# Performance work log

Measured on AMD Instinct MI355X. Metric: run time of the kernel, lower is better.

## Reference

```python
import jax, jax.numpy as jnp
import numpy as np

N_NODES = 50000
N_EDGES = 600000
IN_DIM = 128
HID = 128
OUT_DIM = 2
N_GRAPHS = 64
EPS = 1e-12  # F.normalize default eps


def setup_inputs() -> dict:
    key = jax.random.key(0)
    ks = jax.random.split(key, 16)
    s = 0.05
    x = jax.random.normal(ks[0], (N_NODES, IN_DIM), jnp.float32)
    edge_index = jax.random.randint(ks[1], (2, N_EDGES), 0, N_NODES, dtype=jnp.int32)
    batch = jnp.sort(jax.random.randint(ks[2], (N_NODES,), 0, N_GRAPHS, dtype=jnp.int32))
    # GraphSage layer 0: lin (IN->HID), agg_lin (IN+HID -> HID)
    lin_w0 = jax.random.normal(ks[3], (IN_DIM, HID), jnp.float32) * s
    lin_b0 = jnp.zeros((HID,), jnp.float32)
    agg_w0 = jax.random.normal(ks[4], (HID + IN_DIM, HID), jnp.float32) * s
    agg_b0 = jnp.zeros((HID,), jnp.float32)
    # GraphSage layer 1: lin (HID->HID), agg_lin (2*HID -> HID)
    lin_w1 = jax.random.normal(ks[5], (HID, HID), jnp.float32) * s
    lin_b1 = jnp.zeros((HID,), jnp.float32)
    agg_w1 = jax.random.normal(ks[6], (2 * HID, HID), jnp.float32) * s
    agg_b1 = jnp.zeros((HID,), jnp.float32)
    # post_mp: Linear(HID,HID) -> Dropout -> Linear(HID,OUT)
    mp_w1 = jax.random.normal(ks[7], (HID, HID), jnp.float32) * s
    mp_b1 = jnp.zeros((HID,), jnp.float32)
    mp_w2 = jax.random.normal(ks[8], (HID, OUT_DIM), jnp.float32) * s
    mp_b2 = jnp.zeros((OUT_DIM,), jnp.float32)
    return dict(x=x, edge_index=edge_index, batch=batch,
                lin_w0=lin_w0, lin_b0=lin_b0, agg_w0=agg_w0, agg_b0=agg_b0,
                lin_w1=lin_w1, lin_b1=lin_b1, agg_w1=agg_w1, agg_b1=agg_b1,
                mp_w1=mp_w1, mp_b1=mp_b1, mp_w2=mp_w2, mp_b2=mp_b2)


def sage_layer(x, lin_w, lin_b, agg_w, agg_b, src, dst, num_nodes):
    # message: ReLU(Linear(x_j)) gathered along source nodes  [E, HID]
    msg = jax.nn.relu(x[src] @ lin_w + lin_b)
    # aggr='mean' scatter to target nodes
    summed = jax.ops.segment_sum(msg, dst, num_segments=num_nodes)
    deg = jax.ops.segment_sum(jnp.ones((src.shape[0], 1), x.dtype), dst,
                              num_segments=num_nodes)
    agg = summed / jnp.maximum(deg, 1.0)
    # update: ReLU(Linear([aggr, x])) then L2-normalize rows
    h = jax.nn.relu(jnp.concatenate([agg, x], axis=-1) @ agg_w + agg_b)
    norm = jnp.sqrt(jnp.sum(h * h, axis=1, keepdims=True))
    return h / jnp.maximum(norm, EPS)


def reference(x, edge_index, batch,
              lin_w0, lin_b0, agg_w0, agg_b0,
              lin_w1, lin_b1, agg_w1, agg_b1,
              mp_w1, mp_b1, mp_w2, mp_b2):
    src, dst = edge_index[0], edge_index[1]
    n = x.shape[0]
    h = sage_layer(x, lin_w0, lin_b0, agg_w0, agg_b0, src, dst, n)
    # F.relu is a no-op on the non-negative normalized output; dropout p=0 -> identity
    h = sage_layer(h, lin_w1, lin_b1, agg_w1, agg_b1, src, dst, n)
    # global max pool over graphs
    pooled = jax.ops.segment_max(h, batch, num_segments=N_GRAPHS)
    pooled = jnp.where(jnp.isfinite(pooled), pooled, 0.0)  # guard empty graphs
    # post_mp: Linear -> Dropout(identity) -> Linear
    z = (pooled @ mp_w1 + mp_b1) @ mp_w2 + mp_b2
    return jax.nn.log_softmax(z, axis=1)
```

## Files before the change

### kernel.cpp

```cpp
#include <hip/hip_runtime.h>

__device__ __forceinline__ float bf2f(ushort u) {
    union { uint i; float f; } c; c.i = ((uint)u) << 16; return c.f;
}
__device__ __forceinline__ ushort f2bf(float f) {
    union { float f; uint i; } c; c.f = f;
    uint b = c.i;
    uint r = (b + 0x7fffu + ((b >> 16) & 1u)) >> 16;
    return (ushort)r;
}

typedef __bf16 v8bf __attribute__((ext_vector_type(8)));
typedef float  v4f  __attribute__((ext_vector_type(4)));

__global__ __launch_bounds__(256) void sniff_kernel(const uint* __restrict__ words, int* __restrict__ flag) {
    __shared__ int s[256];
    int t = threadIdx.x;
    int bad = 0;
    for (int i = t; i < 2048; i += 256) {
        uint w = words[i];
        uint exp = (w >> 7) & 0xffu;
        if (exp >= 143u) bad++;
    }
    s[t] = bad;
    __syncthreads();
    for (int o = 128; o; o >>= 1) {
        if (t < o) s[t] += s[t + o];
        __syncthreads();
    }
    if (t == 0) *flag = (s[0] > 64) ? 1 : 0;
}

__device__ __forceinline__ ushort load_conv(const void* src, int i, int isf32) {
    return isf32 ? f2bf(((const float*)src)[i]) : ((const ushort*)src)[i];
}

__global__ __launch_bounds__(256) void convert_x8(const void* __restrict__ src, ushort* __restrict__ dst,
                                                  int n, const int* __restrict__ flag) {
    int idx = blockIdx.x * 256 + threadIdx.x;
    int base = idx * 8;
    if (base + 8 <= n) {
        if (*flag) {
            const float4* s4 = (const float4*)src;
            float4 a = s4[idx * 2], b = s4[idx * 2 + 1];
            union { ushort u[8]; uint4 v; } o;
            o.u[0] = f2bf(a.x); o.u[1] = f2bf(a.y); o.u[2] = f2bf(a.z); o.u[3] = f2bf(a.w);
            o.u[4] = f2bf(b.x); o.u[5] = f2bf(b.y); o.u[6] = f2bf(b.z); o.u[7] = f2bf(b.w);
            *(uint4*)(dst + base) = o.v;
        } else {
            *(uint4*)(dst + base) = ((const uint4*)src)[idx];
        }
    } else {
        int isf = *flag;
        for (int i = base; i < n; i++) dst[i] = load_conv(src, i, isf);
    }
}

struct SmallSrcs { const void* p[8]; };
__global__ __launch_bounds__(256) void convert_small(SmallSrcs s, ushort* __restrict__ dst,
                                                     const int* __restrict__ flag) {
    const int offs[9] = {0, 128, 256, 384, 512, 16896, 17024, 17280, 17282};
    int idx = blockIdx.x * 256 + threadIdx.x;
    if (idx >= 17282) return;
    int seg = 0;
    while (idx >= offs[seg + 1]) seg++;
    dst[idx] = load_conv(s.p[seg], idx - offs[seg], *flag);
}

__global__ __launch_bounds__(256) void transpose_all(
    const void* __restrict__ w0, const void* __restrict__ wa0,
    const void* __restrict__ w1, const void* __restrict__ wa1,
    ushort* __restrict__ t0, ushort* __restrict__ ta0,
    ushort* __restrict__ t1, ushort* __restrict__ ta1,
    const int* __restrict__ flag) {
    int idx = blockIdx.x * 256 + threadIdx.x;
    const void* W; ushort* T; int K; int local;
    if (idx < 16384)      { W = w0;  T = t0;  K = 128; local = idx; }
    else if (idx < 49152) { W = wa0; T = ta0; K = 256; local = idx - 16384; }
    else if (idx < 65536) { W = w1;  T = t1;  K = 128; local = idx - 49152; }
    else                  { W = wa1; T = ta1; K = 256; local = idx - 65536; }
    ushort v = load_conv(W, local, *flag);
    int k = local >> 7;
    int n = local & 127;
    T[(size_t)n * K + k] = v;
}

__global__ __launch_bounds__(256) void count_deg(const int* __restrict__ dst, int* __restrict__ deg, int E) {
    int i = blockIdx.x * 256 + threadIdx.x;
    if (i < E) atomicAdd(&deg[dst[i]], 1);
}

#define SCAN_CHUNK 1024

__global__ __launch_bounds__(256) void chunk_sum_kernel(const int* __restrict__ deg,
                                                        int* __restrict__ csums, int n) {
    __shared__ int s[256];
    int t = threadIdx.x;
    int base = blockIdx.x * SCAN_CHUNK + t * 4;
    int v = 0;
    if (base + 4 <= n) {
        int4 q = *(const int4*)(deg + base);
        v = q.x + q.y + q.z + q.w;
    } else {
        for (int i = base; i < n; i++) v += deg[i];
    }
    s[t] = v;
    __syncthreads();
    for (int o = 128; o; o >>= 1) {
        if (t < o) s[t] += s[t + o];
        __syncthreads();
    }
    if (t == 0) csums[blockIdx.x] = s[0];
}

__global__ __launch_bounds__(256) void scan_phase2(const int* __restrict__ deg,
                                                   const int* __restrict__ csums,
                                                   int* __restrict__ rowptr, int* __restrict__ cursor,
                                                   int n) {
    __shared__ int red[256];
    int t = threadIdx.x, b = blockIdx.x;
    int v = 0;
    for (int i = t; i < b; i += 256) v += csums[i];
    red[t] = v;
    __syncthreads();
    for (int o = 128; o; o >>= 1) {
        if (t < o) red[t] += red[t + o];
        __syncthreads();
    }
    int chunkOff = red[0];
    __syncthreads();
    int base = b * SCAN_CHUNK + t * 4;
    int d0 = 0, d1 = 0, d2 = 0, d3 = 0;
    if (base + 4 <= n) {
        int4 q = *(const int4*)(deg + base);
        d0 = q.x; d1 = q.y; d2 = q.z; d3 = q.w;
    } else {
        if (base < n)     d0 = deg[base];
        if (base + 1 < n) d1 = deg[base + 1];
        if (base + 2 < n) d2 = deg[base + 2];
        if (base + 3 < n) d3 = deg[base + 3];
    }
    int s4 = d0 + d1 + d2 + d3;
    red[t] = s4;
    __syncthreads();
    for (int o = 1; o < 256; o <<= 1) {
        int u = (t >= o) ? red[t - o] : 0;
        __syncthreads();
        red[t] += u;
        __syncthreads();
    }
    int run = chunkOff + red[t] - s4;
    if (base < n)     { rowptr[base]     = run; cursor[base]     = run; run += d0; }
    if (base + 1 < n) { rowptr[base + 1] = run; cursor[base + 1] = run; run += d1; }
    if (base + 2 < n) { rowptr[base + 2] = run; cursor[base + 2] = run; run += d2; }
    if (base + 3 < n) { rowptr[base + 3] = run; cursor[base + 3] = run; run += d3; }
    if (n >= base && n < base + 4) rowptr[n] = run;
}

__global__ __launch_bounds__(256) void fill_kernel(const int* __restrict__ src, const int* __restrict__ dst,
                                                   int* __restrict__ cursor, int* __restrict__ csr_src, int E) {
    int i = blockIdx.x * 256 + threadIdx.x;
    if (i < E) {
        int pos = atomicAdd(&cursor[dst[i]], 1);
        csr_src[pos] = src[i];
    }
}

template <int NSTAGE, bool NORM>
__global__ __launch_bounds__(256) void gemm_kernel(
    const ushort* __restrict__ A0, const ushort* __restrict__ A1,
    const ushort* __restrict__ Bt, const ushort* __restrict__ bias,
    ushort* __restrict__ Cout, int M) {
    __shared__ __bf16 As[128 * 72];
    __shared__ __bf16 Bs[128 * 72];
    const int t = threadIdx.x;
    const int w = t >> 6, lane = t & 63, ln = lane & 15, q = lane >> 4;
    const int blockRow = blockIdx.x * 128;
    const int K = NSTAGE * 128;

    v4f acc[2][8];
#pragma unroll
    for (int i = 0; i < 2; i++)
#pragma unroll
        for (int j = 0; j < 8; j++) acc[i][j] = (v4f){0.f, 0.f, 0.f, 0.f};

    for (int kc = 0; kc < K; kc += 64) {
        const ushort* Ap = (kc < 128) ? A0 : A1;
        int kin = kc & 127;
#pragma unroll
        for (int i = 0; i < 4; i++) {
            int c = i * 256 + t;
            int row = c >> 3, c8 = c & 7;
            int grow = blockRow + row; if (grow >= M) grow = M - 1;
            *(uint4*)&As[row * 72 + c8 * 8] = *(const uint4*)(Ap + (size_t)grow * 128 + kin + c8 * 8);
            *(uint4*)&Bs[row * 72 + c8 * 8] = *(const uint4*)(Bt + (size_t)row * K + kc + c8 * 8);
        }
        __syncthreads();
#pragma unroll
        for (int k0 = 0; k0 < 64; k0 += 32) {
            v8bf a0 = *(const v8bf*)&As[(w * 32 + ln) * 72 + k0 + q * 8];
            v8bf a1 = *(const v8bf*)&As[(w * 32 + 16 + ln) * 72 + k0 + q * 8];
#pragma unroll
            for (int nt = 0; nt < 8; nt++) {
                v8bf b = *(const v8bf*)&Bs[(nt * 16 + ln) * 72 + k0 + q * 8];
                acc[0][nt] = __builtin_amdgcn_mfma_f32_16x16x32_bf16(a0, b, acc[0][nt], 0, 0, 0);
                acc[1][nt] = __builtin_amdgcn_mfma_f32_16x16x32_bf16(a1, b, acc[1][nt], 0, 0, 0);
            }
        }
        __syncthreads();
    }

    float biasf[8];
#pragma unroll
    for (int nt = 0; nt < 8; nt++) biasf[nt] = bf2f(bias[nt * 16 + ln]);

#pragma unroll
    for (int mt = 0; mt < 2; mt++) {
        float v[8][4];
#pragma unroll
        for (int nt = 0; nt < 8; nt++)
#pragma unroll
            for (int r = 0; r < 4; r++) {
                float x = acc[mt][nt][r] + biasf[nt];
                v[nt][r] = x > 0.f ? x : 0.f;
            }
        float inv[4];
        if (NORM) {
#pragma unroll
            for (int r = 0; r < 4; r++) {
                float p = 0.f;
#pragma unroll
                for (int nt = 0; nt < 8; nt++) p += v[nt][r] * v[nt][r];
                p += __shfl_xor(p, 1);
                p += __shfl_xor(p, 2);
                p += __shfl_xor(p, 4);
                p += __shfl_xor(p, 8);
                inv[r] = 1.0f / fmaxf(sqrtf(p), 1e-12f);
            }
        }
        int rowbase = blockRow + w * 32 + mt * 16 + q * 4;
#pragma unroll
        for (int r = 0; r < 4; r++) {
            int grow = rowbase + r;
            if (grow < M) {
#pragma unroll
                for (int nt = 0; nt < 8; nt++) {
                    float x = NORM ? v[nt][r] * inv[r] : v[nt][r];
                    Cout[(size_t)grow * 128 + nt * 16 + ln] = f2bf(x);
                }
            }
        }
    }
}

__global__ __launch_bounds__(256) void aggregate_kernel(
    const ushort* __restrict__ msg, const int* __restrict__ rowptr,
    const int* __restrict__ csr_src, ushort* __restrict__ agg, int n) {
    int wid = (int)((blockIdx.x * 256u + threadIdx.x) >> 6);
    int lane = threadIdx.x & 63;
    if (wid >= n) return;
    int start = rowptr[wid], end = rowptr[wid + 1];
    float a0 = 0.f, a1 = 0.f;
#pragma unroll 4
    for (int j = start; j < end; j++) {
        int s = csr_src[j];
        uint v = *(const uint*)(msg + (size_t)s * 128 + lane * 2);
        a0 += bf2f((ushort)(v & 0xffffu));
        a1 += bf2f((ushort)(v >> 16));
    }
    float inv = 1.0f / fmaxf((float)(end - start), 1.0f);
    uint o = (uint)f2bf(a0 * inv) | ((uint)f2bf(a1 * inv) << 16);
    *(uint*)(agg + (size_t)wid * 128 + lane * 2) = o;
}

__global__ __launch_bounds__(256) void pool_kernel(const ushort* __restrict__ h, const int* __restrict__ batch,
                                                   int* __restrict__ pooled, int n) {
    int d = threadIdx.x & 127;
    int half = threadIdx.x >> 7;
    int start = blockIdx.x * 128;
    int cur_b = -1;
    float cur_max = 0.f;
    for (int i = 0; i < 64; i++) {
        int node = start + half + i * 2;
        if (node >= n) break;
        int b = batch[node];
        float v = bf2f(h[(size_t)node * 128 + d]);
        if (b != cur_b) {
            if (cur_b >= 0) atomicMax(&pooled[cur_b * 128 + d], __float_as_int(cur_max));
            cur_b = b; cur_max = v;
        } else {
            cur_max = fmaxf(cur_max, v);
        }
    }
    if (cur_b >= 0) atomicMax(&pooled[cur_b * 128 + d], __float_as_int(cur_max));
}

__global__ __launch_bounds__(256) void final_kernel(const float* __restrict__ pooled,
                                                    const ushort* __restrict__ small,
                                                    void* __restrict__ out, int G,
                                                    const int* __restrict__ flag) {
    __shared__ float P[128];
    __shared__ float Thalf[128];
    __shared__ float T[128];
    __shared__ float R0[128], R1[128];
    const ushort* w1 = small + 512;
    const ushort* b1 = small + 16896;
    const ushort* w2 = small + 17024;
    const ushort* b2 = small + 17280;
    int g = blockIdx.x;
    int t = threadIdx.x;
    int j = t & 127, half = t >> 7;
    if (t < 128) P[t] = pooled[g * 128 + t];
    __syncthreads();
    float acc = 0.f;
    int k0 = half * 64;
#pragma unroll 8
    for (int k = k0; k < k0 + 64; k++) acc += P[k] * bf2f(w1[k * 128 + j]);
    if (half == 0) Thalf[j] = acc;
    __syncthreads();
    if (half == 1) T[j] = Thalf[j] + acc + bf2f(b1[j]);
    __syncthreads();
    if (t < 128) {
        float tv = T[t];
        R0[t] = tv * bf2f(w2[t * 2]);
        R1[t] = tv * bf2f(w2[t * 2 + 1]);
    }
    __syncthreads();
    for (int o = 64; o; o >>= 1) {
        if (t < o) { R0[t] += R0[t + o]; R1[t] += R1[t + o]; }
        __syncthreads();
    }
    if (t == 0) {
        float z0 = R0[0] + bf2f(b2[0]);
        float z1 = R1[0] + bf2f(b2[1]);
        float m = fmaxf(z0, z1);
        float l = m + logf(expf(z0 - m) + expf(z1 - m));
        float o0 = z0 - l, o1 = z1 - l;
        if (*flag) {
            ((float*)out)[2 * g]     = o0;
            ((float*)out)[2 * g + 1] = o1;
        } else {
            ((ushort*)out)[2 * g]     = f2bf(o0);
            ((ushort*)out)[2 * g + 1] = f2bf(o1);
        }
    }
}

extern "C" void kernel_launch(void* const* d_in, const int* in_sizes, int n_in,
                              void* d_out, int out_size, void* d_ws, size_t ws_size,
                              hipStream_t stream) {
    const void* x      = d_in[0];
    const int*  ei     = (const int*)d_in[1];
    const int*  batch  = (const int*)d_in[2];

    const int N = in_sizes[0] / 128;
    const int E = in_sizes[1] / 2;
    const int G = out_size / 2;
    const int* srcIdx = ei;
    const int* dstIdx = ei + E;

    char* ws = (char*)d_ws;
    size_t off = 0;
    auto alloc = [&](size_t bytes) -> void* {
        off = (off + 255) & ~(size_t)255;
        void* p = ws + off;
        off += bytes;
        return p;
    };
    int*    flag    = (int*)alloc(4);
    int*    deg     = (int*)alloc((size_t)N * 4);
    int*    rowptr  = (int*)alloc((size_t)(N + 1) * 4);
    int*    cursor  = (int*)alloc((size_t)N * 4);
    int*    csr_src = (int*)alloc((size_t)E * 4);
    int*    csums   = (int*)alloc(((size_t)N / SCAN_CHUNK + 2) * 4);
    ushort* Wt0     = (ushort*)alloc(128 * 128 * 2);
    ushort* WtA0    = (ushort*)alloc(256 * 128 * 2);
    ushort* Wt1     = (ushort*)alloc(128 * 128 * 2);
    ushort* WtA1    = (ushort*)alloc(256 * 128 * 2);
    ushort* small   = (ushort*)alloc(17282 * 2);
    ushort* xb      = (ushort*)alloc((size_t)N * 128 * 2);
    ushort* msg     = (ushort*)alloc((size_t)N * 128 * 2);
    ushort* agg     = (ushort*)alloc((size_t)N * 128 * 2);
    ushort* h0      = (ushort*)alloc((size_t)N * 128 * 2);
    int*    pooled  = (int*)alloc((size_t)G * 128 * 4);
    ushort* h1 = msg;

    sniff_kernel<<<1, 256, 0, stream>>>((const uint*)x, flag);
    convert_x8<<<(N * 128 + 2047) / 2048, 256, 0, stream>>>(x, xb, N * 128, flag);
    transpose_all<<<384, 256, 0, stream>>>(d_in[3], d_in[5], d_in[7], d_in[9],
                                           Wt0, WtA0, Wt1, WtA1, flag);
    SmallSrcs ss;
    ss.p[0] = d_in[4];  ss.p[1] = d_in[6];  ss.p[2] = d_in[8];  ss.p[3] = d_in[10];
    ss.p[4] = d_in[11]; ss.p[5] = d_in[12]; ss.p[6] = d_in[13]; ss.p[7] = d_in[14];
    convert_small<<<68, 256, 0, stream>>>(ss, small, flag);

    hipMemsetAsync(deg, 0, (size_t)N * 4, stream);
    int eb = (E + 255) / 256;
    count_deg<<<eb, 256, 0, stream>>>(dstIdx, deg, E);
    int nchunks = (N + SCAN_CHUNK - 1) / SCAN_CHUNK;
    chunk_sum_kernel<<<nchunks, 256, 0, stream>>>(deg, csums, N);
    scan_phase2<<<N / SCAN_CHUNK + 1, 256, 0, stream>>>(deg, csums, rowptr, cursor, N);
    fill_kernel<<<eb, 256, 0, stream>>>(srcIdx, dstIdx, cursor, csr_src, E);

    int gb = (N + 127) / 128;
    int ab = (N + 3) / 4;

    gemm_kernel<1, false><<<gb, 256, 0, stream>>>(xb, xb, Wt0, small + 0, msg, N);
    aggregate_kernel<<<ab, 256, 0, stream>>>(msg, rowptr, csr_src, agg, N);
    gemm_kernel<2, true><<<gb, 256, 0, stream>>>(agg, xb, WtA0, small + 128, h0, N);

    gemm_kernel<1, false><<<gb, 256, 0, stream>>>(h0, h0, Wt1, small + 256, msg, N);
    aggregate_kernel<<<ab, 256, 0, stream>>>(msg, rowptr, csr_src, agg, N);
    gemm_kernel<2, true><<<gb, 256, 0, stream>>>(agg, h0, WtA1, small + 384, h1, N);

    hipMemsetAsync(pooled, 0, (size_t)G * 128 * 4, stream);
    pool_kernel<<<(N + 127) / 128, 256, 0, stream>>>(h1, batch, pooled, N);
    final_kernel<<<G, 256, 0, stream>>>((const float*)pooled, small, d_out, G, flag);
}
```

Measured before the change: 324.3 us.

## Fuse max-pool into final GEMM, vectorize aggregation, merge weight prep kernels

```diff
diff --git a/kernel.cpp b/kernel.cpp
--- a/kernel.cpp
+++ b/kernel.cpp
@@ -2,6 +2,12 @@
 
 __device__ __forceinline__ float bf2f(ushort u) {
     union { uint i; float f; } c; c.i = ((uint)u) << 16; return c.f;
+}
+__device__ __forceinline__ float bf2lo(uint v) {
+    union { uint i; float f; } c; c.i = v << 16; return c.f;
+}
+__device__ __forceinline__ float bf2hi(uint v) {
+    union { uint i; float f; } c; c.i = v & 0xffff0000u; return c.f;
 }
 __device__ __forceinline__ ushort f2bf(float f) {
     union { float f; uint i; } c; c.f = f;
@@ -57,32 +63,32 @@
 }
 
 struct SmallSrcs { const void* p[8]; };
-__global__ __launch_bounds__(256) void convert_small(SmallSrcs s, ushort* __restrict__ dst,
-                                                     const int* __restrict__ flag) {
-    const int offs[9] = {0, 128, 256, 384, 512, 16896, 17024, 17280, 17282};
-    int idx = blockIdx.x * 256 + threadIdx.x;
-    if (idx >= 17282) return;
-    int seg = 0;
-    while (idx >= offs[seg + 1]) seg++;
-    dst[idx] = load_conv(s.p[seg], idx - offs[seg], *flag);
-}
-
-__global__ __launch_bounds__(256) void transpose_all(
+__global__ __launch_bounds__(256) void prep_weights(
     const void* __restrict__ w0, const void* __restrict__ wa0,
     const void* __restrict__ w1, const void* __restrict__ wa1,
     ushort* __restrict__ t0, ushort* __restrict__ ta0,
     ushort* __restrict__ t1, ushort* __restrict__ ta1,
+    SmallSrcs s, ushort* __restrict__ smalldst,
     const int* __restrict__ flag) {
     int idx = blockIdx.x * 256 + threadIdx.x;
-    const void* W; ushort* T; int K; int local;
-    if (idx < 16384)      { W = w0;  T = t0;  K = 128; local = idx; }
-    else if (idx < 49152) { W = wa0; T = ta0; K = 256; local = idx - 16384; }
-    else if (idx < 65536) { W = w1;  T = t1;  K = 128; local = idx - 49152; }
-    else                  { W = wa1; T = ta1; K = 256; local = idx - 65536; }
-    ushort v = load_conv(W, local, *flag);
-    int k = local >> 7;
-    int n = local & 127;
-    T[(size_t)n * K + k] = v;
+    if (idx < 98304) {
+        const void* W; ushort* T; int K; int local;
+        if (idx < 16384)      { W = w0;  T = t0;  K = 128; local = idx; }
+        else if (idx < 49152) { W = wa0; T = ta0; K = 256; local = idx - 16384; }
+        else if (idx < 65536) { W = w1;  T = t1;  K = 128; local = idx - 49152; }
+        else                  { W = wa1; T = ta1; K = 256; local = idx - 65536; }
+        ushort v = load_conv(W, local, *flag);
+        int k = local >> 7;
+        int n = local & 127;
+        T[(size_t)n * K + k] = v;
+    } else {
+        int si = idx - 98304;
+        if (si >= 17282) return;
+        const int offs[9] = {0, 128, 256, 384, 512, 16896, 17024, 17280, 17282};
+        int seg = 0;
+        while (si >= offs[seg + 1]) seg++;
+        smalldst[si] = load_conv(s.p[seg], si - offs[seg], *flag);
+    }
 }
 
 __global__ __launch_bounds__(256) void count_deg(const int* __restrict__ dst, int* __restrict__ deg, int E) {
@@ -166,17 +172,23 @@
     }
 }
 
-template <int NSTAGE, bool NORM>
+template <int NSTAGE, bool NORM, bool POOL>
 __global__ __launch_bounds__(256) void gemm_kernel(
     const ushort* __restrict__ A0, const ushort* __restrict__ A1,
     const ushort* __restrict__ Bt, const ushort* __restrict__ bias,
-    ushort* __restrict__ Cout, int M) {
+    ushort* __restrict__ Cout, int M,
+    const int* __restrict__ batchv, int* __restrict__ pooled) {
     __shared__ __bf16 As[128 * 72];
     __shared__ __bf16 Bs[128 * 72];
+    __shared__ int PoolLoc[POOL ? 8 * 128 : 1];
     const int t = threadIdx.x;
     const int w = t >> 6, lane = t & 63, ln = lane & 15, q = lane >> 4;
     const int blockRow = blockIdx.x * 128;
     const int K = NSTAGE * 128;
+
+    if (POOL) {
+        for (int i = t; i < 8 * 128; i += 256) PoolLoc[i] = 0;
+    }
 
     v4f acc[2][8];
 #pragma unroll
@@ -213,6 +225,8 @@
     float biasf[8];
 #pragma unroll
     for (int nt = 0; nt < 8; nt++) biasf[nt] = bf2f(bias[nt * 16 + ln]);
+
+    const int minB = POOL ? batchv[blockRow < M ? blockRow : M - 1] : 0;
 
 #pragma unroll
     for (int mt = 0; mt < 2; mt++) {
@@ -243,12 +257,35 @@
         for (int r = 0; r < 4; r++) {
             int grow = rowbase + r;
             if (grow < M) {
-#pragma unroll
-                for (int nt = 0; nt < 8; nt++) {
-                    float x = NORM ? v[nt][r] * inv[r] : v[nt][r];
-                    Cout[(size_t)grow * 128 + nt * 16 + ln] = f2bf(x);
+                if (POOL) {
+                    int b = batchv[grow];
+                    int rel = b - minB;
+#pragma unroll
+                    for (int nt = 0; nt < 8; nt++) {
+                        float x = v[nt][r] * inv[r];
+                        int xi = __float_as_int(x);
+                        if (rel < 8) atomicMax(&PoolLoc[rel * 128 + nt * 16 + ln], xi);
+                        else         atomicMax(&pooled[b * 128 + nt * 16 + ln], xi);
+                    }
+                } else {
+#pragma unroll
+                    for (int nt = 0; nt < 8; nt++) {
+                        float x = NORM ? v[nt][r] * inv[r] : v[nt][r];
+                        Cout[(size_t)grow * 128 + nt * 16 + ln] = f2bf(x);
+                    }
                 }
             }
+        }
+    }
+
+    if (POOL) {
+        __syncthreads();
+        int lastRow = blockRow + 127; if (lastRow >= M) lastRow = M - 1;
+        int span = batchv[lastRow] - minB + 1;
+        if (span > 8) span = 8;
+        for (int i = t; i < span * 128; i += 256) {
+            int vv = PoolLoc[i];
+            if (vv != 0) atomicMax(&pooled[(minB + (i >> 7)) * 128 + (i & 127)], vv);
         }
     }
 }
@@ -258,41 +295,32 @@
     const int* __restrict__ csr_src, ushort* __restrict__ agg, int n) {
     int wid = (int)((blockIdx.x * 256u + threadIdx.x) >> 6);
     int lane = threadIdx.x & 63;
+    int sub = lane >> 4;
+    int l16 = lane & 15;
     if (wid >= n) return;
     int start = rowptr[wid], end = rowptr[wid + 1];
-    float a0 = 0.f, a1 = 0.f;
-#pragma unroll 4
-    for (int j = start; j < end; j++) {
+    float a[8] = {0.f, 0.f, 0.f, 0.f, 0.f, 0.f, 0.f, 0.f};
+#pragma unroll 2
+    for (int j = start + sub; j < end; j += 4) {
         int s = csr_src[j];
-        uint v = *(const uint*)(msg + (size_t)s * 128 + lane * 2);
-        a0 += bf2f((ushort)(v & 0xffffu));
-        a1 += bf2f((ushort)(v >> 16));
-    }
-    float inv = 1.0f / fmaxf((float)(end - start), 1.0f);
-    uint o = (uint)f2bf(a0 * inv) | ((uint)f2bf(a1 * inv) << 16);
-    *(uint*)(agg + (size_t)wid * 128 + lane * 2) = o;
-}
-
-__global__ __launch_bounds__(256) void pool_kernel(const ushort* __restrict__ h, const int* __restrict__ batch,
-                                                   int* __restrict__ pooled, int n) {
-    int d = threadIdx.x & 127;
-    int half = threadIdx.x >> 7;
-    int start = blockIdx.x * 128;
-    int cur_b = -1;
-    float cur_max = 0.f;
-    for (int i = 0; i < 64; i++) {
-        int node = start + half + i * 2;
-        if (node >= n) break;
-        int b = batch[node];
-        float v = bf2f(h[(size_t)node * 128 + d]);
-        if (b != cur_b) {
-            if (cur_b >= 0) atomicMax(&pooled[cur_b * 128 + d], __float_as_int(cur_max));
-            cur_b = b; cur_max = v;
-        } else {
-            cur_max = fmaxf(cur_max, v);
-        }
-    }
-    if (cur_b >= 0) atomicMax(&pooled[cur_b * 128 + d], __float_as_int(cur_max));
+        uint4 v = *(const uint4*)(msg + (size_t)s * 128 + l16 * 8);
+        a[0] += bf2lo(v.x); a[1] += bf2hi(v.x);
+        a[2] += bf2lo(v.y); a[3] += bf2hi(v.y);
+        a[4] += bf2lo(v.z); a[5] += bf2hi(v.z);
+        a[6] += bf2lo(v.w); a[7] += bf2hi(v.w);
+    }
+#pragma unroll
+    for (int i = 0; i < 8; i++) {
+        a[i] += __shfl_xor(a[i], 16);
+        a[i] += __shfl_xor(a[i], 32);
+    }
+    if (sub == 0) {
+        float inv = 1.0f / fmaxf((float)(end - start), 1.0f);
+        union { ushort u[8]; uint4 v; } o;
+#pragma unroll
+        for (int i = 0; i < 8; i++) o.u[i] = f2bf(a[i] * inv);
+        *(uint4*)(agg + (size_t)wid * 128 + l16 * 8) = o.v;
+    }
 }
 
 __global__ __launch_bounds__(256) void final_kernel(const float* __restrict__ pooled,
@@ -383,18 +411,17 @@
     ushort* agg     = (ushort*)alloc((size_t)N * 128 * 2);
     ushort* h0      = (ushort*)alloc((size_t)N * 128 * 2);
     int*    pooled  = (int*)alloc((size_t)G * 128 * 4);
-    ushort* h1 = msg;
 
     sniff_kernel<<<1, 256, 0, stream>>>((const uint*)x, flag);
     convert_x8<<<(N * 128 + 2047) / 2048, 256, 0, stream>>>(x, xb, N * 128, flag);
-    transpose_all<<<384, 256, 0, stream>>>(d_in[3], d_in[5], d_in[7], d_in[9],
-                                           Wt0, WtA0, Wt1, WtA1, flag);
     SmallSrcs ss;
     ss.p[0] = d_in[4];  ss.p[1] = d_in[6];  ss.p[2] = d_in[8];  ss.p[3] = d_in[10];
     ss.p[4] = d_in[11]; ss.p[5] = d_in[12]; ss.p[6] = d_in[13]; ss.p[7] = d_in[14];
-    convert_small<<<68, 256, 0, stream>>>(ss, small, flag);
+    prep_weights<<<452, 256, 0, stream>>>(d_in[3], d_in[5], d_in[7], d_in[9],
+                                          Wt0, WtA0, Wt1, WtA1, ss, small, flag);
 
     hipMemsetAsync(deg, 0, (size_t)N * 4, stream);
+    hipMemsetAsync(pooled, 0, (size_t)G * 128 * 4, stream);
     int eb = (E + 255) / 256;
     count_deg<<<eb, 256, 0, stream>>>(dstIdx, deg, E);
     int nchunks = (N + SCAN_CHUNK - 1) / SCAN_CHUNK;
@@ -405,15 +432,13 @@
     int gb = (N + 127) / 128;
     int ab = (N + 3) / 4;
 
-    gemm_kernel<1, false><<<gb, 256, 0, stream>>>(xb, xb, Wt0, small + 0, msg, N);
+    gemm_kernel<1, false, false><<<gb, 256, 0, stream>>>(xb, xb, Wt0, small + 0, msg, N, nullptr, nullptr);
     aggregate_kernel<<<ab, 256, 0, stream>>>(msg, rowptr, csr_src, agg, N);
-    gemm_kernel<2, true><<<gb, 256, 0, stream>>>(agg, xb, WtA0, small + 128, h0, N);
-
-    gemm_kernel<1, false><<<gb, 256, 0, stream>>>(h0, h0, Wt1, small + 256, msg, N);
+    gemm_kernel<2, true, false><<<gb, 256, 0, stream>>>(agg, xb, WtA0, small + 128, h0, N, nullptr, nullptr);
+
+    gemm_kernel<1, false, false><<<gb, 256, 0, stream>>>(h0, h0, Wt1, small + 256, msg, N, nullptr, nullptr);
     aggregate_kernel<<<ab, 256, 0, stream>>>(msg, rowptr, csr_src, agg, N);
-    gemm_kernel<2, true><<<gb, 256, 0, stream>>>(agg, h0, WtA1, small + 384, h1, N);
-
-    hipMemsetAsync(pooled, 0, (size_t)G * 128 * 4, stream);
-    pool_kernel<<<(N + 127) / 128, 256, 0, stream>>>(h1, batch, pooled, N);
+    gemm_kernel<2, true, true><<<gb, 256, 0, stream>>>(agg, h0, WtA1, small + 384, nullptr, N, batch, pooled);
+
     final_kernel<<<G, 256, 0, stream>>>((const float*)pooled, small, d_out, G, flag);
 }
```

Measured after the change: 282.7 us. 1.15x faster.
